# Kernel tuning notes

Hardware: AMD Instinct MI355X
Metric: run time of the kernel (lower is better)

Reference implementation:

```python
import jax, jax.numpy as jnp
import numpy as np

B, IMG_DIM, H, W = 2, 256, 64, 64
PC_C, PC_D = 16, 16          # voxel_dim = PC_C * PC_D = 256
VOXEL_DIM = PC_C * PC_D
QK_DIM = 256                 # out_channels of img_conv / voxel_conv


def _conv1x1(x, w, b):
    # x: [B, Cin, H, W], w: [Cout, Cin], b: [Cout]  (1x1 conv == per-pixel matmul)
    return jnp.einsum('bchw,oc->bohw', x, w) + b[None, :, None, None]


def setup_inputs() -> dict:
    key = jax.random.key(0)
    ks = jax.random.split(key, 10)
    s = 0.02
    return {
        'img': jax.random.normal(ks[0], (B, IMG_DIM, H, W), jnp.float32),
        'pc': jax.random.normal(ks[1], (B, PC_D, H, W, PC_C), jnp.float32),  # dense() layout [B,D,H,W,C]
        'img_conv_w': jax.random.normal(ks[2], (QK_DIM, IMG_DIM), jnp.float32) * s,
        'img_conv_b': jnp.zeros((QK_DIM,), jnp.float32),
        'voxel_conv_w': jax.random.normal(ks[3], (QK_DIM, VOXEL_DIM), jnp.float32) * s,
        'voxel_conv_b': jnp.zeros((QK_DIM,), jnp.float32),
        'img_v_w': jax.random.normal(ks[4], (IMG_DIM, IMG_DIM), jnp.float32) * s,
        'img_v_b': jnp.zeros((IMG_DIM,), jnp.float32),
        'voxel_v_w': jax.random.normal(ks[5], (VOXEL_DIM, VOXEL_DIM), jnp.float32) * s,
        'voxel_v_b': jnp.zeros((VOXEL_DIM,), jnp.float32),
    }


def reference(img, pc, img_conv_w, img_conv_b, voxel_conv_w, voxel_conv_b,
              img_v_w, img_v_b, voxel_v_w, voxel_v_b):
    b, c_img, h, w = img.shape
    # pc.dense() -> permute(0,4,1,2,3) -> [B, C, D, H, W] -> [B, C*D, H, W]
    pc = jnp.transpose(pc, (0, 4, 1, 2, 3))
    pcb, pcc, pcd, pch, pcw = pc.shape
    pc2 = pc.reshape(pcb, pcc * pcd, pch, pcw)
    n = h * w  # == pch * pcw (required by the bmms)

    img_q = _conv1x1(img, img_conv_w, img_conv_b).reshape(b, QK_DIM, n).transpose(0, 2, 1)  # [B, N, 256]
    pc_k = _conv1x1(pc2, voxel_conv_w, voxel_conv_b).reshape(b, QK_DIM, n)                  # [B, 256, N]
    # unscaled single-head cross attention, softmax over voxel positions
    attn = jax.nn.softmax(jnp.einsum('bnc,bcm->bnm', img_q, pc_k), axis=-1)                 # [B, N_img, N_pc]

    img_v = _conv1x1(img, img_v_w, img_v_b).reshape(b, c_img, n)                            # [B, C_img, N]
    img_v = jnp.einsum('bcn,bmn->bcm', img_v, attn).reshape(b, c_img, h, w)                 # img_v @ attn^T

    pc_v = _conv1x1(pc2, voxel_v_w, voxel_v_b).reshape(b, pcc * pcd, n)                     # [B, C*D, N]
    pc_v = jnp.einsum('bcn,bmn->bcm', pc_v, attn).reshape(b, pcc, pcd, pch, pcw)
    return (img_v, pc_v)
```

## Files before the change

kernel.cpp:

```cpp
#include <hip/hip_runtime.h>
#include <hip/hip_bf16.h>


typedef __hip_bfloat16 bf16;
typedef __attribute__((ext_vector_type(8))) short bf16x8;
typedef __attribute__((ext_vector_type(4))) float f32x4;

#define AS1 __attribute__((address_space(1)))
#define AS3 __attribute__((address_space(3)))

__device__ __forceinline__ void gld_lds16(const bf16* g, bf16* s) {
    __builtin_amdgcn_global_load_lds((const AS1 void*)g, (AS3 void*)s, 16, 0, 0);
}

__device__ __forceinline__ bf16x8 cvt8(const float* __restrict__ p) {
    const float4 a = *(const float4*)p;
    const float4 b = *(const float4*)(p + 4);
    bf16 t[8];
    t[0] = __float2bfloat16(a.x); t[1] = __float2bfloat16(a.y);
    t[2] = __float2bfloat16(a.z); t[3] = __float2bfloat16(a.w);
    t[4] = __float2bfloat16(b.x); t[5] = __float2bfloat16(b.y);
    t[6] = __float2bfloat16(b.z); t[7] = __float2bfloat16(b.w);
    return *(const bf16x8*)t;
}

__global__ __launch_bounds__(256) void proj_kernel(
    const float* __restrict__ img, const float* __restrict__ pc,
    const float* __restrict__ Wq,  const float* __restrict__ bq,
    const float* __restrict__ Wk,  const float* __restrict__ bk,
    const float* __restrict__ Wvi, const float* __restrict__ bvi,
    const float* __restrict__ Wvp, const float* __restrict__ bvp,
    bf16* __restrict__ Qw, bf16* __restrict__ Ktw, bf16* __restrict__ Vall)
{
    __shared__ __align__(16) bf16 XT[64][264];

    const int blk = blockIdx.x;
    const int s   = blk >> 8;
    const int b   = (blk >> 7) & 1;
    const int g   = (blk >> 6) & 1;
    const int n0  = (blk & 63) * 64;
    const int tid = threadIdx.x;

    if (s == 0) {
        const float* src = img + b * 1048576;
        for (int k = 0; k < 16; k++) {
            const int i = tid + k * 256;
            const int cin = i >> 4, nl4 = (i & 15) * 4;
            const float4 v = *(const float4*)&src[cin * 4096 + n0 + nl4];
            XT[nl4 + 0][cin] = __float2bfloat16(v.x);
            XT[nl4 + 1][cin] = __float2bfloat16(v.y);
            XT[nl4 + 2][cin] = __float2bfloat16(v.z);
            XT[nl4 + 3][cin] = __float2bfloat16(v.w);
        }
    } else {
        const float* src = pc + b * 1048576;
        for (int k = 0; k < 16; k++) {
            const int d = k, u = tid;
            const int nl = u >> 2, c4 = (u & 3) * 4;
            const float4 v = *(const float4*)&src[d * 65536 + (n0 + nl) * 16 + c4];
            XT[nl][(c4 + 0) * 16 + d] = __float2bfloat16(v.x);
            XT[nl][(c4 + 1) * 16 + d] = __float2bfloat16(v.y);
            XT[nl][(c4 + 2) * 16 + d] = __float2bfloat16(v.z);
            XT[nl][(c4 + 3) * 16 + d] = __float2bfloat16(v.w);
        }
    }
    __syncthreads();

    const float* W = s ? (g ? Wvp : Wk) : (g ? Wvi : Wq);
    const float* Bv = s ? (g ? bvp : bk) : (g ? bvi : bq);

    const int wv = tid >> 6, lane = tid & 63, l16 = lane & 15, quad = lane >> 4;
    const int ob = wv * 64;

    f32x4 acc[4][4] = {};

    for (int ks = 0; ks < 8; ks++) {
        const int k0 = ks * 32;
        bf16x8 af[4], wf[4];
        for (int ti = 0; ti < 4; ti++)
            af[ti] = *(const bf16x8*)&XT[ti * 16 + l16][k0 + quad * 8];
        for (int tj = 0; tj < 4; tj++)
            wf[tj] = cvt8(&W[(ob + tj * 16 + l16) * 256 + k0 + quad * 8]);
        for (int ti = 0; ti < 4; ti++)
            for (int tj = 0; tj < 4; tj++)
                acc[ti][tj] = __builtin_amdgcn_mfma_f32_16x16x32_bf16(af[ti], wf[tj], acc[ti][tj], 0, 0, 0);
    }

    if (g == 0) {
        bf16* D1 = (s ? Ktw : Qw) + b * (4096 * 256);
        for (int tj = 0; tj < 4; tj++) {
            const int o = ob + tj * 16 + l16;
            const float bias = Bv[o];
            for (int ti = 0; ti < 4; ti++) {
                const int nl = ti * 16 + quad * 4;
                for (int r = 0; r < 4; r++)
                    D1[(n0 + nl + r) * 256 + o] = __float2bfloat16(acc[ti][tj][r] + bias);
            }
        }
    } else {
        bf16* D2 = Vall + b * (512 * 4096) + (s ? 256 * 4096 : 0);
        for (int tj = 0; tj < 4; tj++) {
            const int o = ob + tj * 16 + l16;
            const float bias = Bv[o];
            for (int ti = 0; ti < 4; ti++) {
                const int nl = ti * 16 + quad * 4;
                bf16 pv[4];
                for (int r = 0; r < 4; r++)
                    pv[r] = __float2bfloat16(acc[ti][tj][r] + bias);
                *(uint2*)&D2[o * 4096 + n0 + nl] = *(const uint2*)pv;
            }
        }
    }
}

__global__ __launch_bounds__(256) void attn_s_kernel(
    const bf16* __restrict__ Qw, const bf16* __restrict__ Ktw,
    bf16* __restrict__ Pt, float* __restrict__ Lpart)
{
    __shared__ __align__(16) bf16 As[128 * 32];
    __shared__ __align__(16) bf16 Bs[128 * 32];

    const int b  = blockIdx.z;
    const int q0 = blockIdx.y * 128;
    const int p0 = blockIdx.x * 128;
    const bf16* A = Qw  + b * (4096 * 256);
    const bf16* B = Ktw + b * (4096 * 256);

    const int tid = threadIdx.x;
    const int wv = tid >> 6, lane = tid & 63, l16 = lane & 15, quad = lane >> 4;
    const int wr = wv >> 1, wc = wv & 1;

    f32x4 acc[4][4] = {};

    for (int ks = 0; ks < 8; ks++) {
        const int k0 = ks * 32;
        bf16x8 av[2], bv[2];
        for (int c = 0; c < 2; c++) {
            const int ci = c * 256 + tid;
            const int row = ci >> 2, kc = ci & 3;
            av[c] = *(const bf16x8*)&A[(q0 + row) * 256 + k0 + kc * 8];
            bv[c] = *(const bf16x8*)&B[(p0 + row) * 256 + k0 + kc * 8];
        }
        __syncthreads();
        for (int c = 0; c < 2; c++) {
            const int ci = c * 256 + tid;
            *(bf16x8*)&As[ci * 8] = av[c];
            *(bf16x8*)&Bs[ci * 8] = bv[c];
        }
        __syncthreads();
        bf16x8 af[4], bfr[4];
        for (int t = 0; t < 4; t++) {
            af[t]  = *(const bf16x8*)&As[(wr * 64 + t * 16 + l16) * 32 + quad * 8];
            bfr[t] = *(const bf16x8*)&Bs[(wc * 64 + t * 16 + l16) * 32 + quad * 8];
        }
        for (int ti = 0; ti < 4; ti++)
            for (int tj = 0; tj < 4; tj++)
                acc[ti][tj] = __builtin_amdgcn_mfma_f32_16x16x32_bf16(af[ti], bfr[tj], acc[ti][tj], 0, 0, 0);
    }

    bf16* Pdst = Pt + (size_t)b * 4096 * 4096;
    const int strip = blockIdx.x * 2 + wc;
    for (int ti = 0; ti < 4; ti++) {
        for (int r = 0; r < 4; r++) {
            const int qrow = wr * 64 + ti * 16 + quad * 4 + r;
            const int q = q0 + qrow;
            float partial = 0.0f;
            for (int tj = 0; tj < 4; tj++) {
                const float e = __expf(fminf(acc[ti][tj][r], 80.0f));
                partial += e;
                Pdst[(size_t)q * 4096 + p0 + wc * 64 + tj * 16 + l16] = __float2bfloat16(e);
            }
            partial += __shfl_xor(partial, 1);
            partial += __shfl_xor(partial, 2);
            partial += __shfl_xor(partial, 4);
            partial += __shfl_xor(partial, 8);
            if (l16 == 0)
                Lpart[(size_t)(b * 4096 + q) * 64 + strip] = partial;
        }
    }
}

__global__ __launch_bounds__(256) void lred_kernel(
    const float* __restrict__ Lpart, float* __restrict__ Linv)
{
    const int row = blockIdx.x * 256 + threadIdx.x;
    const float4* lp = (const float4*)&Lpart[(size_t)row * 64];
    float s = 0.0f;
    for (int i = 0; i < 16; i++) {
        const float4 v = lp[i];
        s += v.x + v.y + v.z + v.w;
    }
    Linv[row] = 1.0f / fmaxf(s, 1e-30f);
}

__global__ __launch_bounds__(1024, 8) void attn_o_kernel(
    const bf16* __restrict__ Vall, const bf16* __restrict__ Pt,
    const float* __restrict__ Linv, float* __restrict__ out)
{
    __shared__ __align__(16) bf16 smem[4][6144];

    const int b  = blockIdx.z;
    const int c0 = blockIdx.y * 128;
    const int q0 = blockIdx.x * 64;
    const bf16* A = Vall + (size_t)b * 512 * 4096;
    const bf16* B = Pt   + (size_t)b * 4096 * 4096;

    const int tid = threadIdx.x;
    const int grp = tid >> 8;
    const int t8  = tid & 255;
    const int wv = t8 >> 6, lane = t8 & 63, l16 = lane & 15, quad = lane >> 4;
    const int wr = wv >> 1, wc = wv & 1;

    bf16* As = smem[grp];
    bf16* Bs = smem[grp] + 4096;

    int aoff[4], boff[2];
    for (int t = 0; t < 4; t++) {
        const int row = wr * 64 + t * 16 + l16;
        aoff[t] = row * 32 + (quad ^ ((row >> 1) & 3)) * 8;
    }
    for (int t = 0; t < 2; t++) {
        const int row = wc * 32 + t * 16 + l16;
        boff[t] = row * 32 + (quad ^ ((row >> 1) & 3)) * 8;
    }

    const int arow = t8 >> 2;
    const int kswz = ((t8 & 3) ^ ((arow >> 1) & 3)) * 8;

    f32x4 acc[4][2] = {};

    for (int ks = 0; ks < 32; ks++) {
        const int k0 = grp * 1024 + ks * 32 + kswz;
        gld_lds16(A + (c0 + arow) * 4096 + k0, As + t8 * 8);
        gld_lds16(A + (c0 + 64 + arow) * 4096 + k0, As + 2048 + t8 * 8);
        gld_lds16(B + (q0 + arow) * 4096 + k0, Bs + t8 * 8);
        __syncthreads();
        bf16x8 af[4], bfr[2];
        for (int t = 0; t < 4; t++) af[t]  = *(const bf16x8*)&As[aoff[t]];
        for (int t = 0; t < 2; t++) bfr[t] = *(const bf16x8*)&Bs[boff[t]];
        for (int ti = 0; ti < 4; ti++)
            for (int tj = 0; tj < 2; tj++)
                acc[ti][tj] = __builtin_amdgcn_mfma_f32_16x16x32_bf16(af[ti], bfr[tj], acc[ti][tj], 0, 0, 0);
        __syncthreads();
    }

    float* comb = (float*)&smem[0][0];
    const int sl0 = (wr * 64 + quad * 4) * 64 + wc * 32 + l16;
    if (grp == 0) {
        for (int ti = 0; ti < 4; ti++)
            for (int tj = 0; tj < 2; tj++)
                for (int r = 0; r < 4; r++)
                    comb[sl0 + (ti * 16 + r) * 64 + tj * 16] = acc[ti][tj][r];
    }
    __syncthreads();
    for (int g = 1; g < 4; g++) {
        if (grp == g) {
            for (int ti = 0; ti < 4; ti++)
                for (int tj = 0; tj < 2; tj++)
                    for (int r = 0; r < 4; r++)
                        comb[sl0 + (ti * 16 + r) * 64 + tj * 16] += acc[ti][tj][r];
        }
        __syncthreads();
    }

    const int f0 = tid * 8;
    const int cl = f0 >> 6, ql = f0 & 63;
    const int c_ = c0 + cl;
    const size_t base = (c_ < 256)
        ? ((size_t)b * 1048576 + (size_t)c_ * 4096)
        : (2097152u + (size_t)b * 1048576 + (size_t)(c_ - 256) * 4096);
    const float4 v0 = *(const float4*)&comb[f0];
    const float4 v1 = *(const float4*)&comb[f0 + 4];
    const float4 l0 = *(const float4*)&Linv[b * 4096 + q0 + ql];
    const float4 l1 = *(const float4*)&Linv[b * 4096 + q0 + ql + 4];
    float4 o0, o1;
    o0.x = v0.x * l0.x; o0.y = v0.y * l0.y; o0.z = v0.z * l0.z; o0.w = v0.w * l0.w;
    o1.x = v1.x * l1.x; o1.y = v1.y * l1.y; o1.z = v1.z * l1.z; o1.w = v1.w * l1.w;
    *(float4*)&out[base + q0 + ql]     = o0;
    *(float4*)&out[base + q0 + ql + 4] = o1;
}

extern "C" void kernel_launch(void* const* d_in, const int* in_sizes, int n_in,
                              void* d_out, int out_size, void* d_ws, size_t ws_size,
                              hipStream_t stream)
{
    const float* img = (const float*)d_in[0];
    const float* pc  = (const float*)d_in[1];
    const float* Wq  = (const float*)d_in[2];
    const float* bq  = (const float*)d_in[3];
    const float* Wk  = (const float*)d_in[4];
    const float* bk  = (const float*)d_in[5];
    const float* Wvi = (const float*)d_in[6];
    const float* bvi = (const float*)d_in[7];
    const float* Wvp = (const float*)d_in[8];
    const float* bvp = (const float*)d_in[9];

    char* ws = (char*)d_ws;
    bf16*  Qw    = (bf16*)(ws);
    bf16*  Ktw   = (bf16*)(ws + (4ull  << 20));
    bf16*  Vall  = (bf16*)(ws + (8ull  << 20));
    bf16*  Pt    = (bf16*)(ws + (16ull << 20));
    float* Lpart = (float*)(ws + (80ull << 20));
    float* Linv  = (float*)(ws + (82ull << 20));

    proj_kernel<<<512, 256, 0, stream>>>(img, pc, Wq, bq, Wk, bk,
                                         Wvi, bvi, Wvp, bvp, Qw, Ktw, Vall);
    attn_s_kernel<<<dim3(32, 32, 2), 256, 0, stream>>>(Qw, Ktw, Pt, Lpart);
    lred_kernel<<<32, 256, 0, stream>>>(Lpart, Linv);
    attn_o_kernel<<<dim3(64, 4, 2), 1024, 0, stream>>>(Vall, Pt, Linv, (float*)d_out);
}
```

Baseline: 202.7 us.

## Double-buffer attn_o LDS loads and halve split-K groups per block

The attn_o kernel drops from four to two split-K thread groups per block (512 threads). Each group now walks twice as many K steps with double-buffered LDS staging: the next tile's global-to-LDS loads are issued before the current tile's MFMAs, using explicit vmcnt waits and raw barriers. It also raises wave priority around the MFMA block and shortens the cross-group reduction to a single accumulate step. The aim is to hide global load latency and reduce reduction and sync overhead, at the cost of fewer threads per block and longer serial K loops.

Result: no change. 202.3 us (-0.2%).

```diff
diff --git a/kernel.cpp b/kernel.cpp
--- a/kernel.cpp
+++ b/kernel.cpp
@@ -193,11 +193,11 @@
     Linv[row] = 1.0f / fmaxf(s, 1e-30f);
 }
 
-__global__ __launch_bounds__(1024, 8) void attn_o_kernel(
+__global__ __launch_bounds__(512, 4) void attn_o_kernel(
     const bf16* __restrict__ Vall, const bf16* __restrict__ Pt,
     const float* __restrict__ Linv, float* __restrict__ out)
 {
-    __shared__ __align__(16) bf16 smem[4][6144];
+    __shared__ __align__(16) bf16 smem[2][2][6144];
 
     const int b  = blockIdx.z;
     const int c0 = blockIdx.y * 128;
@@ -211,9 +211,6 @@
     const int wv = t8 >> 6, lane = t8 & 63, l16 = lane & 15, quad = lane >> 4;
     const int wr = wv >> 1, wc = wv & 1;
 
-    bf16* As = smem[grp];
-    bf16* Bs = smem[grp] + 4096;
-
     int aoff[4], boff[2];
     for (int t = 0; t < 4; t++) {
         const int row = wr * 64 + t * 16 + l16;
@@ -226,23 +223,51 @@
 
     const int arow = t8 >> 2;
     const int kswz = ((t8 & 3) ^ ((arow >> 1) & 3)) * 8;
+    const bf16* Ag0 = A + (c0 + arow) * 4096 + grp * 2048 + kswz;
+    const bf16* Ag1 = A + (c0 + 64 + arow) * 4096 + grp * 2048 + kswz;
+    const bf16* Bg  = B + (q0 + arow) * 4096 + grp * 2048 + kswz;
 
     f32x4 acc[4][2] = {};
 
-    for (int ks = 0; ks < 32; ks++) {
-        const int k0 = grp * 1024 + ks * 32 + kswz;
-        gld_lds16(A + (c0 + arow) * 4096 + k0, As + t8 * 8);
-        gld_lds16(A + (c0 + 64 + arow) * 4096 + k0, As + 2048 + t8 * 8);
-        gld_lds16(B + (q0 + arow) * 4096 + k0, Bs + t8 * 8);
-        __syncthreads();
+#define STAGE(buf, ks)                                                  \
+    do {                                                                \
+        const int _k = (ks) * 32;                                       \
+        bf16* _s = &smem[grp][(buf)][0];                                \
+        gld_lds16(Ag0 + _k, _s + t8 * 8);                               \
+        gld_lds16(Ag1 + _k, _s + 2048 + t8 * 8);                        \
+        gld_lds16(Bg  + _k, _s + 4096 + t8 * 8);                        \
+    } while (0)
+
+    STAGE(0, 0);
+    int cur = 0;
+    for (int ks = 0; ks < 64; ks++) {
+        if (ks + 1 < 64) {
+            STAGE(cur ^ 1, ks + 1);
+            asm volatile("s_waitcnt vmcnt(3)" ::: "memory");
+        } else {
+            asm volatile("s_waitcnt vmcnt(0)" ::: "memory");
+        }
+        __builtin_amdgcn_s_barrier();
+        __builtin_amdgcn_sched_barrier(0);
+
+        const bf16* As_ = &smem[grp][cur][0];
+        const bf16* Bs_ = &smem[grp][cur][4096];
         bf16x8 af[4], bfr[2];
-        for (int t = 0; t < 4; t++) af[t]  = *(const bf16x8*)&As[aoff[t]];
-        for (int t = 0; t < 2; t++) bfr[t] = *(const bf16x8*)&Bs[boff[t]];
+        for (int t = 0; t < 4; t++) af[t]  = *(const bf16x8*)&As_[aoff[t]];
+        for (int t = 0; t < 2; t++) bfr[t] = *(const bf16x8*)&Bs_[boff[t]];
+        __builtin_amdgcn_s_setprio(1);
         for (int ti = 0; ti < 4; ti++)
             for (int tj = 0; tj < 2; tj++)
                 acc[ti][tj] = __builtin_amdgcn_mfma_f32_16x16x32_bf16(af[ti], bfr[tj], acc[ti][tj], 0, 0, 0);
-        __syncthreads();
-    }
+        __builtin_amdgcn_s_setprio(0);
+
+        asm volatile("s_waitcnt lgkmcnt(0)" ::: "memory");
+        __builtin_amdgcn_s_barrier();
+        cur ^= 1;
+    }
+#undef STAGE
+
+    __syncthreads();
 
     float* comb = (float*)&smem[0][0];
     const int sl0 = (wr * 64 + quad * 4) * 64 + wc * 32 + l16;
@@ -253,31 +278,27 @@
                     comb[sl0 + (ti * 16 + r) * 64 + tj * 16] = acc[ti][tj][r];
     }
     __syncthreads();
-    for (int g = 1; g < 4; g++) {
-        if (grp == g) {
-            for (int ti = 0; ti < 4; ti++)
-                for (int tj = 0; tj < 2; tj++)
-                    for (int r = 0; r < 4; r++)
-                        comb[sl0 + (ti * 16 + r) * 64 + tj * 16] += acc[ti][tj][r];
-        }
-        __syncthreads();
-    }
-
-    const int f0 = tid * 8;
+    if (grp == 1) {
+        for (int ti = 0; ti < 4; ti++)
+            for (int tj = 0; tj < 2; tj++)
+                for (int r = 0; r < 4; r++)
+                    comb[sl0 + (ti * 16 + r) * 64 + tj * 16] += acc[ti][tj][r];
+    }
+    __syncthreads();
+
+    const int f0 = tid * 16;
     const int cl = f0 >> 6, ql = f0 & 63;
     const int c_ = c0 + cl;
     const size_t base = (c_ < 256)
         ? ((size_t)b * 1048576 + (size_t)c_ * 4096)
         : (2097152u + (size_t)b * 1048576 + (size_t)(c_ - 256) * 4096);
-    const float4 v0 = *(const float4*)&comb[f0];
-    const float4 v1 = *(const float4*)&comb[f0 + 4];
-    const float4 l0 = *(const float4*)&Linv[b * 4096 + q0 + ql];
-    const float4 l1 = *(const float4*)&Linv[b * 4096 + q0 + ql + 4];
-    float4 o0, o1;
-    o0.x = v0.x * l0.x; o0.y = v0.y * l0.y; o0.z = v0.z * l0.z; o0.w = v0.w * l0.w;
-    o1.x = v1.x * l1.x; o1.y = v1.y * l1.y; o1.z = v1.z * l1.z; o1.w = v1.w * l1.w;
-    *(float4*)&out[base + q0 + ql]     = o0;
-    *(float4*)&out[base + q0 + ql + 4] = o1;
+    for (int j = 0; j < 4; j++) {
+        const float4 v = *(const float4*)&comb[f0 + j * 4];
+        const float4 l = *(const float4*)&Linv[b * 4096 + q0 + ql + j * 4];
+        float4 o;
+        o.x = v.x * l.x; o.y = v.y * l.y; o.z = v.z * l.z; o.w = v.w * l.w;
+        *(float4*)&out[base + q0 + ql + j * 4] = o;
+    }
 }
 
 extern "C" void kernel_launch(void* const* d_in, const int* in_sizes, int n_in,
@@ -307,5 +328,5 @@
                                          Wvi, bvi, Wvp, bvp, Qw, Ktw, Vall);
     attn_s_kernel<<<dim3(32, 32, 2), 256, 0, stream>>>(Qw, Ktw, Pt, Lpart);
     lred_kernel<<<32, 256, 0, stream>>>(Lpart, Linv);
-    attn_o_kernel<<<dim3(64, 4, 2), 1024, 0, stream>>>(Vall, Pt, Linv, (float*)d_out);
-}
+    attn_o_kernel<<<dim3(64, 4, 2), 512, 0, stream>>>(Vall, Pt, Linv, (float*)d_out);
+}
```
